# Kernel tuning notes

Measured on AMD Instinct MI355X. Metric: run time of the kernel, lower is better.

## Reference

```python
import jax, jax.numpy as jnp
import numpy as np


def reference(x, weight, bias):
    """Per-sample dynamic conv2d, expressed as one grouped convolution.

    x:      (B, C_in, H, W)
    weight: (B, C_out, C_in, kH, kW)
    bias:   (B, C_out)
    returns (B, C_out, H_out, W_out) with H_out = H - kH + 1 (valid conv)
    """
    B, C_in, H, W = x.shape
    C_out, kH, kW = weight.shape[1], weight.shape[3], weight.shape[4]
    # Fold batch into channels: groups=B grouped conv == B independent convs.
    x_g = x.reshape(1, B * C_in, H, W)
    w_g = weight.reshape(B * C_out, C_in, kH, kW)
    out = jax.lax.conv_general_dilated(
        x_g, w_g,
        window_strides=(1, 1),
        padding='VALID',
        dimension_numbers=('NCHW', 'OIHW', 'NCHW'),
        feature_group_count=B,
    )  # (1, B*C_out, H_out, W_out)
    out = out.reshape(B, C_out, out.shape[2], out.shape[3])
    return out + bias[:, :, None, None]


def setup_inputs() -> dict:
    key = jax.random.key(0)
    k1, k2, k3 = jax.random.split(key, 3)
    B, C_in, C_out, H, W, kH, kW = 16, 64, 64, 128, 128, 3, 3
    x = jax.random.normal(k1, (B, C_in, H, W), dtype=jnp.float32)
    weight = jax.random.normal(k2, (B, C_out, C_in, kH, kW), dtype=jnp.float32) * 0.05
    bias = jax.random.normal(k3, (B, C_out), dtype=jnp.float32)
    return {"x": x, "weight": weight, "bias": bias}
```

## Files before the change

kernel.cpp:

```cpp
#include <hip/hip_runtime.h>

#define BATCH 16
#define CI 64
#define CO 64
#define H 128
#define W 128
#define HO 126
#define WO 126

typedef short bfrag __attribute__((ext_vector_type(8)));
typedef float ffrag __attribute__((ext_vector_type(4)));

#define AS3(p) ((__attribute__((address_space(3))) void*)(p))
#define AS1(p) ((const __attribute__((address_space(1))) void*)(p))

static __device__ __forceinline__ unsigned short f2bf(float f) {
    unsigned u = __float_as_uint(f);
    u += 0x7fffu + ((u >> 16) & 1u);
    return (unsigned short)(u >> 16);
}

__global__ void wt_prepass(const float* __restrict__ w, unsigned short* __restrict__ w_t) {
    int i = blockIdx.x * 256 + threadIdx.x;
    int ci = i & 63;
    int co = (i >> 6) & 63;
    int bs = i >> 12;
    int b = bs / 9, s = bs - b * 9;
    w_t[i] = f2bf(w[(((b * 64 + co) * 64 + ci) * 9) + s]);
}

__global__ void xt_prepass(const float* __restrict__ x, unsigned short* __restrict__ x_tg) {
    __shared__ float tile[64 * 32 * 4];
    const int tid = threadIdx.x;
    const int y = blockIdx.x;
    const int b = blockIdx.y;

    const float* xp = x + (size_t)b * CI * H * W + (size_t)y * W;
    #pragma unroll
    for (int p = 0; p < 8; ++p) {
        int item = p * 256 + tid;
        int colq = item & 31;
        int ci   = item >> 5;
        float4 v = *(const float4*)(xp + (size_t)ci * H * W + colq * 4);
        int slot = colq ^ (ci >> 3);
        *(float4*)&tile[(ci * 32 + slot) * 4] = v;
    }
    __syncthreads();

    unsigned short* og = x_tg + ((size_t)(b * 128 + y)) * 1024 * 8;
    #pragma unroll
    for (int q = 0; q < 4; ++q) {
        int item = q * 256 + tid;
        int o   = item & 7;
        int col = item >> 3;
        unsigned short u[8];
        #pragma unroll
        for (int e = 0; e < 8; ++e) {
            int ci = o * 8 + e;
            u[e] = f2bf(tile[(ci * 32 + ((col >> 2) ^ o)) * 4 + (col & 3)]);
        }
        int chunk = col * 8 + (o ^ (col & 7));
        *(uint4*)&og[chunk * 8] = *(const uint4*)u;
    }
}

__launch_bounds__(256, 2)
__global__ void dynconv_mfma(const unsigned short* __restrict__ x_tg,
                             const unsigned short* __restrict__ w_t,
                             const float* __restrict__ bias,
                             float* __restrict__ out) {
    __shared__ __align__(16) unsigned short xs[4 * 8192];

    const int tid  = threadIdx.x;
    const int rg   = blockIdx.x;
    const int b    = blockIdx.y;
    const int y0   = rg * 2;
    const int wave = tid >> 6;
    const int lane = tid & 63;
    const int l16  = lane & 15;
    const int lq   = lane >> 4;
    const int wm   = wave & 1;
    const int wn   = wave >> 1;

    {
        const unsigned short* gsrc = x_tg + ((size_t)(b * 128 + y0 + wave)) * 8192;
        #pragma unroll
        for (int i = 0; i < 16; ++i) {
            __builtin_amdgcn_global_load_lds(AS1(gsrc + i * 512 + lane * 8),
                                             AS3(xs + wave * 8192 + i * 512),
                                             16, 0, 0);
        }
    }

    const bfrag* wtb = (const bfrag*)w_t + (size_t)(b * 9) * 512;
    const int co_b = wm * 32 + l16;
    bfrag acur[4], anxt[4];
    #pragma unroll
    for (int ks = 0; ks < 2; ++ks)
        #pragma unroll
        for (int mt = 0; mt < 2; ++mt)
            acur[ks * 2 + mt] = wtb[(co_b + mt * 16) * 8 + ks * 4 + lq];

    ffrag acc[2][8];
    #pragma unroll
    for (int mt = 0; mt < 2; ++mt)
        #pragma unroll
        for (int nt = 0; nt < 8; ++nt)
            acc[mt][nt] = (ffrag){0.f, 0.f, 0.f, 0.f};

    __syncthreads();

    for (int s = 0; s < 9; ++s) {
        if (s < 8) {
            const bfrag* wn2 = wtb + (s + 1) * 512;
            #pragma unroll
            for (int ks = 0; ks < 2; ++ks)
                #pragma unroll
                for (int mt = 0; mt < 2; ++mt)
                    anxt[ks * 2 + mt] = wn2[(co_b + mt * 16) * 8 + ks * 4 + lq];
        }
        const int dy = s / 3, dx = s - dy * 3;
        const int xr = wn + dy;
        #pragma unroll
        for (int ks = 0; ks < 2; ++ks) {
            const int o = ks * 4 + lq;
            #pragma unroll
            for (int nt = 0; nt < 8; ++nt) {
                int colx = nt * 16 + l16 + dx;
                if (colx > 127) colx = 127;
                const bfrag bf = *(const bfrag*)&xs[xr * 8192 + (colx * 8 + (o ^ (colx & 7))) * 8];
                acc[0][nt] = __builtin_amdgcn_mfma_f32_16x16x32_bf16(acur[ks * 2 + 0], bf, acc[0][nt], 0, 0, 0);
                acc[1][nt] = __builtin_amdgcn_mfma_f32_16x16x32_bf16(acur[ks * 2 + 1], bf, acc[1][nt], 0, 0, 0);
            }
        }
        #pragma unroll
        for (int j = 0; j < 4; ++j) acur[j] = anxt[j];
    }

    const int oy = y0 + wn;
    #pragma unroll
    for (int mt = 0; mt < 2; ++mt) {
        #pragma unroll
        for (int r = 0; r < 4; ++r) {
            int co = wm * 32 + mt * 16 + lq * 4 + r;
            float bv = bias[b * 64 + co];
            float* op = out + ((size_t)(b * 64 + co) * HO + oy) * WO;
            #pragma unroll
            for (int nt = 0; nt < 8; ++nt) {
                int ox = nt * 16 + l16;
                if (ox < WO) op[ox] = acc[mt][nt][r] + bv;
            }
        }
    }
}

extern "C" void kernel_launch(void* const* d_in, const int* in_sizes, int n_in,
                              void* d_out, int out_size, void* d_ws, size_t ws_size,
                              hipStream_t stream) {
    const float* x    = (const float*)d_in[0];
    const float* w    = (const float*)d_in[1];
    const float* bias = (const float*)d_in[2];
    float* out        = (float*)d_out;

    unsigned short* w_t  = (unsigned short*)d_ws;
    unsigned short* x_tg = (unsigned short*)((char*)d_ws + 1179648);

    wt_prepass<<<dim3(589824 / 256), dim3(256), 0, stream>>>(w, w_t);
    xt_prepass<<<dim3(128, BATCH), dim3(256), 0, stream>>>(x, x_tg);
    dynconv_mfma<<<dim3(63, BATCH), dim3(256), 0, stream>>>(x_tg, w_t, bias, out);
}
```

Before: 151.9 us.

## Fuse input bf16 transpose prepass into the MFMA conv kernel

Removes the separate x transpose/convert kernel and has each conv block load its 4 input rows directly from fp32 x, converting to bf16 and writing the swizzled channel-interleaved layout into LDS. This drops a kernel launch and the round trip of the bf16 intermediate through global memory. In exchange, input rows are read twice by adjacent row-group blocks (halo overlap), async global-to-LDS loads become synchronous per-thread loads with conversion in the critical path, and the strided channel loads are scalar.

```diff
diff --git a/kernel.cpp b/kernel.cpp
--- a/kernel.cpp
+++ b/kernel.cpp
@@ -1,4 +1,5 @@
 #include <hip/hip_runtime.h>
+#include <hip/hip_bf16.h>
 
 #define BATCH 16
 #define CI 64
@@ -10,9 +11,6 @@
 
 typedef short bfrag __attribute__((ext_vector_type(8)));
 typedef float ffrag __attribute__((ext_vector_type(4)));
-
-#define AS3(p) ((__attribute__((address_space(3))) void*)(p))
-#define AS1(p) ((const __attribute__((address_space(1))) void*)(p))
 
 static __device__ __forceinline__ unsigned short f2bf(float f) {
     unsigned u = __float_as_uint(f);
@@ -29,46 +27,11 @@
     w_t[i] = f2bf(w[(((b * 64 + co) * 64 + ci) * 9) + s]);
 }
 
-__global__ void xt_prepass(const float* __restrict__ x, unsigned short* __restrict__ x_tg) {
-    __shared__ float tile[64 * 32 * 4];
-    const int tid = threadIdx.x;
-    const int y = blockIdx.x;
-    const int b = blockIdx.y;
-
-    const float* xp = x + (size_t)b * CI * H * W + (size_t)y * W;
-    #pragma unroll
-    for (int p = 0; p < 8; ++p) {
-        int item = p * 256 + tid;
-        int colq = item & 31;
-        int ci   = item >> 5;
-        float4 v = *(const float4*)(xp + (size_t)ci * H * W + colq * 4);
-        int slot = colq ^ (ci >> 3);
-        *(float4*)&tile[(ci * 32 + slot) * 4] = v;
-    }
-    __syncthreads();
-
-    unsigned short* og = x_tg + ((size_t)(b * 128 + y)) * 1024 * 8;
-    #pragma unroll
-    for (int q = 0; q < 4; ++q) {
-        int item = q * 256 + tid;
-        int o   = item & 7;
-        int col = item >> 3;
-        unsigned short u[8];
-        #pragma unroll
-        for (int e = 0; e < 8; ++e) {
-            int ci = o * 8 + e;
-            u[e] = f2bf(tile[(ci * 32 + ((col >> 2) ^ o)) * 4 + (col & 3)]);
-        }
-        int chunk = col * 8 + (o ^ (col & 7));
-        *(uint4*)&og[chunk * 8] = *(const uint4*)u;
-    }
-}
-
 __launch_bounds__(256, 2)
-__global__ void dynconv_mfma(const unsigned short* __restrict__ x_tg,
-                             const unsigned short* __restrict__ w_t,
-                             const float* __restrict__ bias,
-                             float* __restrict__ out) {
+__global__ void dynconv_fused(const float* __restrict__ x,
+                              const unsigned short* __restrict__ w_t,
+                              const float* __restrict__ bias,
+                              float* __restrict__ out) {
     __shared__ __align__(16) unsigned short xs[4 * 8192];
 
     const int tid  = threadIdx.x;
@@ -83,12 +46,25 @@
     const int wn   = wave >> 1;
 
     {
-        const unsigned short* gsrc = x_tg + ((size_t)(b * 128 + y0 + wave)) * 8192;
+        const int col = tid & 127;
+        const int h   = tid >> 7;
+        const float* xb = x + (size_t)b * CI * H * W + (size_t)y0 * W + col;
         #pragma unroll
-        for (int i = 0; i < 16; ++i) {
-            __builtin_amdgcn_global_load_lds(AS1(gsrc + i * 512 + lane * 8),
-                                             AS3(xs + wave * 8192 + i * 512),
-                                             16, 0, 0);
+        for (int row = 0; row < 4; ++row) {
+            #pragma unroll
+            for (int oc = 0; oc < 4; ++oc) {
+                const int o = h * 4 + oc;
+                const float* p = xb + (size_t)(o * 8) * (H * W) + row * W;
+                unsigned int u[4];
+                #pragma unroll
+                for (int e = 0; e < 4; ++e) {
+                    float f0 = p[(size_t)(2 * e) * (H * W)];
+                    float f1 = p[(size_t)(2 * e + 1) * (H * W)];
+                    __hip_bfloat162 h2 = __float22bfloat162_rn(make_float2(f0, f1));
+                    u[e] = *(unsigned int*)&h2;
+                }
+                *(uint4*)&xs[(row * 1024 + col * 8 + (o ^ (col & 7))) * 8] = *(const uint4*)u;
+            }
         }
     }
 
@@ -162,10 +138,8 @@
     const float* bias = (const float*)d_in[2];
     float* out        = (float*)d_out;
 
-    unsigned short* w_t  = (unsigned short*)d_ws;
-    unsigned short* x_tg = (unsigned short*)((char*)d_ws + 1179648);
+    unsigned short* w_t = (unsigned short*)d_ws;
 
     wt_prepass<<<dim3(589824 / 256), dim3(256), 0, stream>>>(w, w_t);
-    xt_prepass<<<dim3(128, BATCH), dim3(256), 0, stream>>>(x, x_tg);
-    dynconv_mfma<<<dim3(63, BATCH), dim3(256), 0, stream>>>(x_tg, w_t, bias, out);
+    dynconv_fused<<<dim3(63, BATCH), dim3(256), 0, stream>>>(x, w_t, bias, out);
 }
```

After: 141.4 us. 6.9% less time.
